# Optimization experiments

Measured on AMD Instinct MI355X. Metric: run time of the kernel, lower is better.

Reference implementation:

```python
import jax, jax.numpy as jnp
import numpy as np

B, L, DIN, H, N, TEMB, NB = 16, 1024, 64, 256, 64, 128, 6


def setup_inputs() -> dict:
    key = jax.random.key(0)
    ks = jax.random.split(key, 16)
    def nrm(k, shape, scale):
        return jax.random.normal(k, shape, dtype=jnp.float32) * scale
    inp = {}
    inp["input"] = nrm(ks[0], (B, L, DIN), 1.0)
    inp["t"] = jax.random.uniform(ks[1], (B,), dtype=jnp.float32) * 1000.0
    inp["W_in"] = nrm(ks[2], (DIN, H), DIN ** -0.5)
    inp["b_in"] = jnp.zeros((H,), jnp.float32)
    inp["Wt1"] = nrm(ks[3], (TEMB, H), TEMB ** -0.5)
    inp["bt1"] = jnp.zeros((H,), jnp.float32)
    inp["Wt2"] = nrm(ks[4], (H, H), H ** -0.5)
    inp["bt2"] = jnp.zeros((H,), jnp.float32)
    inp["ln_g"] = jnp.ones((NB, H), jnp.float32)
    inp["ln_b"] = jnp.zeros((NB, H), jnp.float32)
    lo, hi = float(np.log(0.001)), float(np.log(0.1))
    inp["log_dt"] = jax.random.uniform(ks[5], (NB, H), dtype=jnp.float32) * (hi - lo) + lo
    inp["A_log_re"] = jnp.full((NB, H, N), float(np.log(0.5)), jnp.float32)
    inp["A_im"] = jnp.broadcast_to(np.pi * jnp.arange(N, dtype=jnp.float32), (NB, H, N)) + 0.0
    inp["C_re"] = nrm(ks[6], (NB, 2, H, N), 0.5 ** 0.5)
    inp["C_im"] = nrm(ks[7], (NB, 2, H, N), 0.5 ** 0.5)
    inp["Dp"] = nrm(ks[8], (NB, H), 1.0)
    inp["s4W"] = nrm(ks[9], (NB, H, H), H ** -0.5)
    inp["s4b"] = jnp.zeros((NB, H), jnp.float32)
    inp["tW"] = nrm(ks[10], (NB, H, H), H ** -0.5)
    inp["tb"] = jnp.zeros((NB, H), jnp.float32)
    inp["c1W"] = nrm(ks[11], (NB, H, H), H ** -0.5)
    inp["c1b"] = jnp.zeros((NB, H), jnp.float32)
    inp["c2W"] = nrm(ks[12], (NB, H, H), H ** -0.5)
    inp["c2b"] = jnp.zeros((NB, H), jnp.float32)
    inp["Wo1"] = nrm(ks[13], (H, H), H ** -0.5)
    inp["bo1"] = jnp.zeros((H,), jnp.float32)
    inp["Wo2"] = nrm(ks[14], (H, DIN), H ** -0.5)
    inp["bo2"] = jnp.zeros((DIN,), jnp.float32)
    return inp


def _sin_emb(t, dim):
    half = dim // 2
    freqs = jnp.exp(-np.log(10000.0) / (half - 1) * jnp.arange(half, dtype=jnp.float32))
    a = t[:, None] * freqs[None, :]
    return jnp.concatenate([jnp.sin(a), jnp.cos(a)], axis=-1)


def _forward(input, t, W_in, b_in, Wt1, bt1, Wt2, bt2, ln_g, ln_b, log_dt, A_log_re,
             A_im, C_re, C_im, Dp, s4W, s4b, tW, tb, c1W, c1b, c2W, c2b, Wo1, bo1, Wo2, bo2):
    x = jax.nn.relu(input @ W_in + b_in)                     # [B,L,H]
    tv = jax.nn.silu(_sin_emb(t, TEMB) @ Wt1 + bt1)
    tv = jax.nn.silu(tv @ Wt2 + bt2)                         # [B,H]
    x = jnp.swapaxes(x, -1, -2)                              # [B,H,L]
    length = x.shape[-1]
    nfft = 2 * length
    lgrid = jnp.arange(length)
    skips = jnp.zeros_like(x)
    for i in range(NB):
        # time conditioning (broadcast over L)
        tt = tv @ tW[i] + tb[i]                              # [B,H]
        z = x + tt[:, :, None]
        # LayerNorm over channel dim H
        zt = jnp.swapaxes(z, -1, -2)                         # [B,L,H]
        mu = zt.mean(-1, keepdims=True)
        var = zt.var(-1, keepdims=True)
        zn = (zt - mu) / jnp.sqrt(var + 1e-5) * ln_g[i] + ln_b[i]
        zn = jnp.swapaxes(zn, -1, -2)                        # [B,H,L]
        # S4 (diagonal ZOH) bidirectional convolution kernel
        dt = jnp.exp(log_dt[i])                              # [H]
        A = -jnp.exp(A_log_re[i]) + 1j * A_im[i]             # [H,N]
        dtA = A * dt[:, None]
        C = C_re[i] + 1j * C_im[i]                           # [2,H,N]
        dC = C * (jnp.exp(dtA) - 1.0) / A
        V = jnp.exp(dtA[:, :, None] * lgrid)                 # [H,N,L] Vandermonde
        K = 2.0 * jnp.einsum('shn,hnl->shl', dC, V).real     # [2,H,L]
        k = jnp.pad(K[0], ((0, 0), (0, length))) + jnp.pad(K[1][:, ::-1], ((0, 0), (length, 0)))
        y = jnp.fft.irfft(jnp.fft.rfft(zn, nfft) * jnp.fft.rfft(k, nfft)[None], nfft)[..., :length]
        y = y + zn * Dp[i][None, :, None]
        y = jax.nn.gelu(y, approximate=False)
        y = jnp.einsum('oh,bhl->bol', s4W[i], y) + s4b[i][None, :, None]
        out = y + z                                          # S4Layer residual
        g = jnp.tanh(out) * jax.nn.sigmoid(out)
        x = jnp.einsum('oh,bhl->bol', c1W[i], g) + c1b[i][None, :, None] + x
        skips = skips + jnp.einsum('oh,bhl->bol', c2W[i], g) + c2b[i][None, :, None]
    skip = jnp.swapaxes(skips, -1, -2)                       # [B,L,H]
    h = jax.nn.relu(skip @ Wo1 + bo1)
    out = h @ Wo2 + bo2
    return out + input                                       # init_skip


def reference(input, t, W_in, b_in, Wt1, bt1, Wt2, bt2, ln_g, ln_b, log_dt, A_log_re,
              A_im, C_re, C_im, Dp, s4W, s4b, tW, tb, c1W, c1b, c2W, c2b, Wo1, bo1, Wo2, bo2):
    return _forward(input, t, W_in, b_in, Wt1, bt1, Wt2, bt2, ln_g, ln_b, log_dt, A_log_re,
                    A_im, C_re, C_im, Dp, s4W, s4b, tW, tb, c1W, c1b, c2W, c2b, Wo1, bo1, Wo2, bo2)
```

## Files before the change

### kernel.cpp

```cpp
#include <hip/hip_runtime.h>
#include <math.h>


typedef __attribute__((ext_vector_type(8))) short bf16x8;
typedef __attribute__((ext_vector_type(4))) float f32x4;

__device__ __forceinline__ short f2bf(float f) {
  unsigned u = __builtin_bit_cast(unsigned, f);
  unsigned r = (u + 0x7FFFu + ((u >> 16) & 1u)) >> 16;
  return (short)r;
}
__device__ __forceinline__ float bf2f(unsigned short v) {
  unsigned u = ((unsigned)v) << 16;
  return __builtin_bit_cast(float, u);
}

__global__ __launch_bounds__(256) void k_temb(
    const float* __restrict__ t, const float* __restrict__ Wt1, const float* __restrict__ bt1,
    const float* __restrict__ Wt2, const float* __restrict__ bt2, float* __restrict__ tv) {
  int b = blockIdx.x, tid = threadIdx.x;
  __shared__ float emb[128];
  __shared__ float tv1[256];
  if (tid < 128) {
    int j = tid & 63;
    float f = expf(-logf(10000.f) / 63.f * (float)j);
    float a = t[b] * f;
    emb[tid] = (tid < 64) ? sinf(a) : cosf(a);
  }
  __syncthreads();
  float acc = bt1[tid];
  for (int k = 0; k < 128; k++) acc = fmaf(emb[k], Wt1[k * 256 + tid], acc);
  tv1[tid] = acc / (1.f + expf(-acc));
  __syncthreads();
  float acc2 = bt2[tid];
  for (int k = 0; k < 256; k++) acc2 = fmaf(tv1[k], Wt2[k * 256 + tid], acc2);
  tv[b * 256 + tid] = acc2 / (1.f + expf(-acc2));
}

__global__ __launch_bounds__(256) void k_tt(
    const float* __restrict__ tv, const float* __restrict__ tW, const float* __restrict__ tb,
    float* __restrict__ tt_all) {
  int i = blockIdx.x, b = blockIdx.y, h = threadIdx.x;
  __shared__ float s[256];
  s[h] = tv[b * 256 + h];
  __syncthreads();
  const float* W = tW + i * 256 * 256;
  float acc = tb[i * 256 + h];
  for (int k = 0; k < 256; k++) acc = fmaf(s[k], W[k * 256 + h], acc);
  tt_all[(i * 16 + b) * 256 + h] = acc;
}

__global__ __launch_bounds__(256) void k_in(
    const float* __restrict__ inp, const float* __restrict__ W, const float* __restrict__ bias,
    unsigned short* __restrict__ xbf) {
  int lt = blockIdx.x, b = blockIdx.y, h = threadIdx.x;
  __shared__ float si[64][68];
  int l0 = lt * 64;
  for (int rep = 0; rep < 16; rep++) {
    int idx = rep * 256 + h;
    int l = idx >> 6, d = idx & 63;
    si[l][d] = inp[(size_t)(b * 1024 + l0 + l) * 64 + d];
  }
  float wc[64];
  #pragma unroll
  for (int d = 0; d < 64; d++) wc[d] = W[d * 256 + h];
  float bh = bias[h];
  __syncthreads();
  unsigned short* xp = xbf + (size_t)(b * 256 + h) * 1024 + l0;
  for (int l4 = 0; l4 < 16; l4++) {
    float op[4];
    #pragma unroll
    for (int j = 0; j < 4; j++) {
      int l = l4 * 4 + j;
      float a = bh;
      #pragma unroll
      for (int d4 = 0; d4 < 16; d4++) {
        float4 v = *reinterpret_cast<const float4*>(&si[l][d4 * 4]);
        a = fmaf(v.x, wc[d4 * 4 + 0], a);
        a = fmaf(v.y, wc[d4 * 4 + 1], a);
        a = fmaf(v.z, wc[d4 * 4 + 2], a);
        a = fmaf(v.w, wc[d4 * 4 + 3], a);
      }
      op[j] = fmaxf(a, 0.f);
    }
    ushort4 o = make_ushort4((unsigned short)f2bf(op[0]), (unsigned short)f2bf(op[1]),
                             (unsigned short)f2bf(op[2]), (unsigned short)f2bf(op[3]));
    *reinterpret_cast<ushort4*>(xp + l4 * 4) = o;
  }
}

__global__ __launch_bounds__(256) void k_tab(
    const float* __restrict__ log_dt, const float* __restrict__ A_log_re, const float* __restrict__ A_im,
    const float* __restrict__ C_re, const float* __restrict__ C_im,
    float* __restrict__ wtab, float* __restrict__ wTtab, float* __restrict__ dCtab) {
  int idx = blockIdx.x * 256 + threadIdx.x;
  int i = idx / (256 * 64);
  int rem = idx % (256 * 64);
  int h = rem >> 6, n = rem & 63;
  float dt = expf(log_dt[i * 256 + h]);
  float Ar = -expf(A_log_re[idx]);
  float Ai = A_im[idx];
  float ar = dt * Ar, ai = dt * Ai;
  float ea = expf(ar);
  float wr = ea * cosf(ai), wi = ea * sinf(ai);
  float pr = wr, pi = wi;
  #pragma unroll
  for (int s = 0; s < 6; s++) { float nr = pr * pr - pi * pi; float ni = 2.f * pr * pi; pr = nr; pi = ni; }
  float den = Ar * Ar + Ai * Ai;
  float qr = ((wr - 1.f) * Ar + wi * Ai) / den;
  float qi = (wi * Ar - (wr - 1.f) * Ai) / den;
  wtab[idx * 2] = wr; wtab[idx * 2 + 1] = wi;
  wTtab[idx * 2] = pr; wTtab[idx * 2 + 1] = pi;
  #pragma unroll
  for (int s = 0; s < 2; s++) {
    float cr = C_re[((size_t)(i * 2 + s) * 256 + h) * 64 + n];
    float ci = C_im[((size_t)(i * 2 + s) * 256 + h) * 64 + n];
    dCtab[(((size_t)(i * 2 + s) * 256 + h) * 64 + n) * 2]     = cr * qr - ci * qi;
    dCtab[(((size_t)(i * 2 + s) * 256 + h) * 64 + n) * 2 + 1] = cr * qi + ci * qr;
  }
}

__global__ __launch_bounds__(256) void k_prep(
    const float* __restrict__ s4W, const float* __restrict__ c1W, const float* __restrict__ c2W,
    const float* __restrict__ Wo1,
    unsigned short* __restrict__ s4Wbf, unsigned short* __restrict__ c12Wbf, unsigned short* __restrict__ Wo1T) {
  int idx = blockIdx.x * 256 + threadIdx.x;
  if (idx < 393216) {
    s4Wbf[idx] = (unsigned short)f2bf(s4W[idx]);
  } else if (idx < 393216 + 786432) {
    int j = idx - 393216;
    int i = j / 131072, r = j % 131072;
    int o2 = r >> 8, k = r & 255;
    float v = (o2 < 256) ? c1W[(size_t)i * 65536 + o2 * 256 + k]
                         : c2W[(size_t)i * 65536 + (o2 - 256) * 256 + k];
    c12Wbf[j] = (unsigned short)f2bf(v);
  } else {
    int j = idx - 1179648;
    int o = j >> 8, k = j & 255;
    Wo1T[j] = (unsigned short)f2bf(Wo1[k * 256 + o]);
  }
}

__global__ __launch_bounds__(256) void k_pcar(const float* __restrict__ wtab, unsigned short* __restrict__ Ptb) {
  int idx = blockIdx.x * 256 + threadIdx.x;
  int i = idx >> 14, h = (idx >> 6) & 255, n = idx & 63;
  float wr = wtab[idx * 2], wi = wtab[idx * 2 + 1];
  float pr = 1.f, pi = 0.f;
  unsigned short* base = Ptb + (size_t)i * 2097152 + (size_t)h * 8192 + 2 * n;
  for (int t = 0; t < 64; t++) {
    *reinterpret_cast<ushort2*>(base + t * 128) =
        make_ushort2((unsigned short)f2bf(pr), (unsigned short)f2bf(-pi));
    float nr2 = pr * wr - pi * wi, ni2 = pr * wi + pi * wr;
    pr = nr2; pi = ni2;
  }
}

__global__ __launch_bounds__(256) void k_ktap(
    const float* __restrict__ dCtab, const unsigned short* __restrict__ Ptb, float* __restrict__ Ktap) {
  int idx = blockIdx.x * 256 + threadIdx.x;
  int j = idx & 63;
  int h = (idx >> 6) & 255;
  int i = idx >> 15;
  const float* dc = dCtab + (size_t)(idx >> 6) * 128;
  const unsigned short* P = Ptb + (size_t)i * 2097152 + (size_t)h * 8192 + j * 128;
  float acc = 0.f;
  for (int q = 0; q < 32; q++) {
    float4 d = *reinterpret_cast<const float4*>(dc + q * 4);
    ushort4 p = *reinterpret_cast<const ushort4*>(P + q * 4);
    acc = fmaf(d.x, bf2f(p.x), fmaf(d.y, bf2f(p.y), fmaf(d.z, bf2f(p.z), fmaf(d.w, bf2f(p.w), acc))));
  }
  Ktap[idx] = 2.f * acc;
}

__global__ __launch_bounds__(256) void k_ln(
    const unsigned short* __restrict__ xbf, const float* __restrict__ tt_all,
    const float* __restrict__ g, const float* __restrict__ bta, unsigned short* __restrict__ znbf, int i) {
  int ct = blockIdx.x, b = blockIdx.y, tid = threadIdx.x;
  __shared__ unsigned short tile[64][266];
  __shared__ float stt[256];
  __shared__ float red[8][64];
  __shared__ float mu_s[64], rs_s[64];
  stt[tid] = tt_all[(i * 16 + b) * 256 + tid];
  __syncthreads();
  int l0 = ct * 64;
  const unsigned short* xb = xbf + (size_t)(b * 256) * 1024 + l0;
  for (int rep = 0; rep < 16; rep++) {
    int idx = rep * 256 + tid;
    int h = idx >> 4;
    int l4 = (idx & 15) * 4;
    ushort4 v = *reinterpret_cast<const ushort4*>(xb + (size_t)h * 1024 + l4);
    float a = stt[h];
    tile[l4][h]     = (unsigned short)f2bf(bf2f(v.x) + a);
    tile[l4 + 1][h] = (unsigned short)f2bf(bf2f(v.y) + a);
    tile[l4 + 2][h] = (unsigned short)f2bf(bf2f(v.z) + a);
    tile[l4 + 3][h] = (unsigned short)f2bf(bf2f(v.w) + a);
  }
  __syncthreads();
  int l = tid & 63, part = tid >> 6;
  float s1 = 0.f, s2 = 0.f;
  for (int k = 0; k < 64; k++) {
    float v = bf2f(tile[l][part * 64 + k]);
    s1 += v; s2 = fmaf(v, v, s2);
  }
  red[part][l] = s1; red[4 + part][l] = s2;
  __syncthreads();
  if (tid < 64) {
    float a = red[0][tid] + red[1][tid] + red[2][tid] + red[3][tid];
    float q = red[4][tid] + red[5][tid] + red[6][tid] + red[7][tid];
    float mu = a * (1.f / 256.f);
    float var = q * (1.f / 256.f) - mu * mu;
    mu_s[tid] = mu;
    rs_s[tid] = rsqrtf(var + 1e-5f);
  }
  __syncthreads();
  unsigned short* zb = znbf + (size_t)(b * 256) * 1024 + l0;
  for (int rep = 0; rep < 16; rep++) {
    int idx = rep * 256 + tid;
    int h = idx >> 4;
    int l4 = (idx & 15) * 4;
    float gg = g[i * 256 + h], bb2 = bta[i * 256 + h];
    float o0 = (bf2f(tile[l4][h])     - mu_s[l4])     * rs_s[l4]     * gg + bb2;
    float o1 = (bf2f(tile[l4 + 1][h]) - mu_s[l4 + 1]) * rs_s[l4 + 1] * gg + bb2;
    float o2 = (bf2f(tile[l4 + 2][h]) - mu_s[l4 + 2]) * rs_s[l4 + 2] * gg + bb2;
    float o3 = (bf2f(tile[l4 + 3][h]) - mu_s[l4 + 3]) * rs_s[l4 + 3] * gg + bb2;
    ushort4 o4 = make_ushort4((unsigned short)f2bf(o0), (unsigned short)f2bf(o1),
                              (unsigned short)f2bf(o2), (unsigned short)f2bf(o3));
    *reinterpret_cast<ushort4*>(zb + (size_t)h * 1024 + l4) = o4;
  }
}

__global__ __launch_bounds__(512, 1) void k_s4(
    const unsigned short* __restrict__ znbf, const unsigned short* __restrict__ Ptb,
    const float* __restrict__ wtab, const float* __restrict__ wTtab, const float* __restrict__ dCtab,
    const float* __restrict__ Ktap, const float* __restrict__ Dp,
    unsigned short* __restrict__ ygbf, int i) {
  int h = blockIdx.x;
  int tid = threadIdx.x;
  __shared__ unsigned short Psb[64 * 132];
  __shared__ unsigned short XR[22016];
  __shared__ unsigned short Sw[34816];
  __shared__ float k0s[64], k1s[64];

  if (tid < 64) k0s[tid] = Ktap[h * 64 + tid];
  else if (tid < 128) k1s[tid - 64] = Ktap[16384 + h * 64 + (tid - 64)];

  {
    const unsigned short* src = Ptb + (size_t)h * 8192;
    #pragma unroll
    for (int rep = 0; rep < 4; rep++) {
      int idx4 = (rep * 512 + tid) * 4;
      int t = idx4 >> 7, k = idx4 & 127;
      ushort4 v = *reinterpret_cast<const ushort4*>(src + idx4);
      *reinterpret_cast<ushort4*>(&Psb[t * 132 + k]) = v;
    }
  }
  __syncthreads();
  {
    int t = tid & 63;
    int colblk = tid >> 6;
    #pragma unroll
    for (int cc = 0; cc < 32; cc++) {
      int col = colblk * 32 + cc;
      int n = col & 63, comp = (col >> 6) & 1, dir = col >> 7;
      int k = 2 * n + comp;
      unsigned short v = dir ? Psb[t * 132 + k] : Psb[(63 - t) * 132 + k];
      if (comp) v ^= 0x8000u;
      XR[col * 72 + t] = v;
    }
  }
  __syncthreads();

  int wid = tid >> 6, lane = tid & 63;
  int b = blockIdx.y * 8 + wid;
  int c = lane & 15, kq = lane >> 4;
  const unsigned short* pzn = znbf + ((size_t)(b * 256 + h)) * 1024 + c * 64 + kq * 8;

  bf16x8 af0 = *reinterpret_cast<const bf16x8*>(pzn);
  bf16x8 af1 = *reinterpret_cast<const bf16x8*>(pzn + 32);

  f32x4 acc[16];
  #pragma unroll
  for (int nt = 0; nt < 16; nt++) acc[nt] = (f32x4){0.f, 0.f, 0.f, 0.f};
  #pragma unroll
  for (int nt = 0; nt < 16; nt++) {
    bf16x8 b0 = *reinterpret_cast<const bf16x8*>(&XR[(nt * 16 + c) * 72 + kq * 8]);
    acc[nt] = __builtin_amdgcn_mfma_f32_16x16x32_bf16(af0, b0, acc[nt], 0, 0, 0);
  }
  #pragma unroll
  for (int nt = 0; nt < 16; nt++) {
    bf16x8 b1 = *reinterpret_cast<const bf16x8*>(&XR[(nt * 16 + c) * 72 + 32 + kq * 8]);
    acc[nt] = __builtin_amdgcn_mfma_f32_16x16x32_bf16(af1, b1, acc[nt], 0, 0, 0);
  }
  __syncthreads();

  {
    int trow = tid >> 6, klane = tid & 63;
    #pragma unroll
    for (int ti = 0; ti < 8; ti++) {
      int t2 = ti * 8 + trow;
      #pragma unroll
      for (int kc = 0; kc < 5; kc++) {
        int k = kc * 64 + klane;
        unsigned short v;
        if (kc < 2)      v = Psb[t2 * 132 + k];
        else if (kc < 4) v = Psb[(63 - t2) * 132 + (k - 128)];
        else {
          int tp = klane;
          float f = (t2 >= tp) ? k0s[t2 - tp] : k1s[tp - t2 - 1];
          v = (unsigned short)f2bf(f);
        }
        XR[t2 * 344 + k] = v;
      }
    }
  }

  unsigned short* swf = &Sw[(wid * 2 + 0) * 2176];
  unsigned short* swb = &Sw[(wid * 2 + 1) * 2176];
  const int gib = (i * 256 + h) * 64;
  #pragma unroll
  for (int j = 0; j < 4; j++) {
    int n = j * 16 + c;
    int gi = gib + n;
    float wTr = wTtab[gi * 2], wTi = wTtab[gi * 2 + 1];
    float w2r = wTr * wTr - wTi * wTi, w2i = 2.f * wTr * wTi;
    float w4r = w2r * w2r - w2i * w2i, w4i = 2.f * w2r * w2i;
    float w8r = w4r * w4r - w4i * w4i, w8i = 2.f * w4r * w4i;
    float wr = wtab[gi * 2], wi = wtab[gi * 2 + 1];
    float d0r = dCtab[((size_t)(i * 2 + 0) * 256 + h) * 128 + 2 * n];
    float d0i = dCtab[((size_t)(i * 2 + 0) * 256 + h) * 128 + 2 * n + 1];
    float d1r = dCtab[((size_t)(i * 2 + 1) * 256 + h) * 128 + 2 * n];
    float d1i = dCtab[((size_t)(i * 2 + 1) * 256 + h) * 128 + 2 * n + 1];
    float mfr = 2.f * (d0r * wr - d0i * wi), mfi = 2.f * (d0r * wi + d0i * wr);
    float mbr = 2.f * d1r, mbi = 2.f * d1i;

    {
      float er = 0.f, ei = 0.f, entr[4], enti[4];
      #pragma unroll
      for (int r = 0; r < 4; r++) {
        entr[r] = er; enti[r] = ei;
        float br = acc[j][r], bi = acc[j + 4][r];
        float t0 = er * wTr - ei * wTi + br;
        ei = er * wTi + ei * wTr + bi; er = t0;
      }
      float Gr = er, Gi = ei;
      float sr = __shfl_up(Gr, 16), si = __shfl_up(Gi, 16);
      if (kq >= 1) { Gr += sr * w4r - si * w4i; Gi += sr * w4i + si * w4r; }
      sr = __shfl_up(Gr, 32); si = __shfl_up(Gi, 32);
      if (kq >= 2) { Gr += sr * w8r - si * w8i; Gi += sr * w8i + si * w8r; }
      float Sgr = __shfl_up(Gr, 16), Sgi = __shfl_up(Gi, 16);
      if (kq == 0) { Sgr = 0.f; Sgi = 0.f; }
      float pr = 1.f, pi = 0.f;
      #pragma unroll
      for (int r = 0; r < 4; r++) {
        float scr = pr * Sgr - pi * Sgi + entr[r];
        float sci = pr * Sgi + pi * Sgr + enti[r];
        float opr = mfr * scr - mfi * sci;
        float opi = mfr * sci + mfi * scr;
        *reinterpret_cast<ushort2*>(swf + (kq * 4 + r) * 136 + 2 * n) =
            make_ushort2((unsigned short)f2bf(opr), (unsigned short)f2bf(opi));
        float t0 = pr * wTr - pi * wTi; pi = pr * wTi + pi * wTr; pr = t0;
      }
    }
    {
      float er = 0.f, ei = 0.f, entr[4], enti[4];
      #pragma unroll
      for (int rr = 0; rr < 4; rr++) {
        int r = 3 - rr;
        entr[r] = er; enti[r] = ei;
        float br = acc[8 + j][r], bi = acc[12 + j][r];
        float t0 = er * wTr - ei * wTi + br;
        ei = er * wTi + ei * wTr + bi; er = t0;
      }
      float Gr = er, Gi = ei;
      float sr = __shfl_down(Gr, 16), si = __shfl_down(Gi, 16);
      if (kq <= 2) { Gr += sr * w4r - si * w4i; Gi += sr * w4i + si * w4r; }
      sr = __shfl_down(Gr, 32); si = __shfl_down(Gi, 32);
      if (kq <= 1) { Gr += sr * w8r - si * w8i; Gi += sr * w8i + si * w8r; }
      float Sgr = __shfl_down(Gr, 16), Sgi = __shfl_down(Gi, 16);
      if (kq == 3) { Sgr = 0.f; Sgi = 0.f; }
      float pr = 1.f, pi = 0.f;
      #pragma unroll
      for (int rr = 0; rr < 4; rr++) {
        int r = 3 - rr;
        float scr = pr * Sgr - pi * Sgi + entr[r];
        float sci = pr * Sgi + pi * Sgr + enti[r];
        float opr = mbr * scr - mbi * sci;
        float opi = mbr * sci + mbi * scr;
        *reinterpret_cast<ushort2*>(swb + (kq * 4 + r) * 136 + 2 * n) =
            make_ushort2((unsigned short)f2bf(opr), (unsigned short)f2bf(opi));
        float t0 = pr * wTr - pi * wTi; pi = pr * wTi + pi * wTr; pr = t0;
      }
    }
  }
  __syncthreads();

  f32x4 acc2[4];
  #pragma unroll
  for (int nt = 0; nt < 4; nt++) acc2[nt] = (f32x4){0.f, 0.f, 0.f, 0.f};
  #pragma unroll
  for (int ks = 0; ks < 10; ks++) {
    bf16x8 af;
    if (ks < 4)       af = *reinterpret_cast<const bf16x8*>(swf + c * 136 + ks * 32 + kq * 8);
    else if (ks < 8)  af = *reinterpret_cast<const bf16x8*>(swb + c * 136 + (ks - 4) * 32 + kq * 8);
    else              af = *reinterpret_cast<const bf16x8*>(pzn + (ks - 8) * 32);
    #pragma unroll
    for (int nt = 0; nt < 4; nt++) {
      bf16x8 bfv = *reinterpret_cast<const bf16x8*>(&XR[(nt * 16 + c) * 344 + ks * 32 + kq * 8]);
      acc2[nt] = __builtin_amdgcn_mfma_f32_16x16x32_bf16(af, bfv, acc2[nt], 0, 0, 0);
    }
  }

  float dp = Dp[i * 256 + h];
  size_t obase = (size_t)(b * 256 + h) * 1024;
  #pragma unroll
  for (int nt = 0; nt < 4; nt++) {
    #pragma unroll
    for (int r = 0; r < 4; r++) {
      int m = kq * 4 + r;
      int t = nt * 16 + c;
      size_t idx = obase + (size_t)m * 64 + t;
      float z = bf2f(znbf[idx]);
      float v = fmaf(z, dp, acc2[nt][r]);
      float gel = 0.5f * v * (1.f + erff(v * 0.70710678118f));
      ygbf[idx] = (unsigned short)f2bf(gel);
    }
  }
}

template <int EPI>
__global__ __launch_bounds__(256) void k_gemm(
    const unsigned short* __restrict__ Wbf, const float* __restrict__ bias1, const float* __restrict__ bias2,
    const unsigned short* __restrict__ act, unsigned short* __restrict__ uio1, unsigned short* __restrict__ uio2,
    unsigned short* __restrict__ outb, const unsigned short* __restrict__ aux1, const float* __restrict__ aux2) {
  int lt = blockIdx.x, ot = blockIdx.y, b = blockIdx.z;
  int tid = threadIdx.x;
  int l0 = lt * 128, o0 = ot * 64;
  __shared__ unsigned short Alds[128 * 40];

  int wid = tid >> 6, lane = tid & 63;
  int wo = wid >> 1, wl = wid & 1;
  int c = lane & 15, kq = lane >> 4;

  int kq4 = tid >> 5;
  int lq = tid & 31;
  const unsigned short* actb = act + (size_t)(b * 256) * 1024 + l0 + lq * 4;

  f32x4 acc[2][4];
  #pragma unroll
  for (int mo = 0; mo < 2; mo++)
    #pragma unroll
    for (int nl = 0; nl < 4; nl++) acc[mo][nl] = (f32x4){0.f, 0.f, 0.f, 0.f};

  ushort4 m0, m1, m2, m3;
  {
    const unsigned short* p = actb + (size_t)(kq4 * 4) * 1024;
    m0 = *reinterpret_cast<const ushort4*>(p);
    m1 = *reinterpret_cast<const ushort4*>(p + 1024);
    m2 = *reinterpret_cast<const ushort4*>(p + 2048);
    m3 = *reinterpret_cast<const ushort4*>(p + 3072);
  }

  for (int kc = 0; kc < 256; kc += 32) {
    {
      int g0 = kq4 >> 1, hh = (kq4 & 1) * 4;
      int rot = (g0 + lq) & 3;
      unsigned short* wp = &Alds[(lq * 4) * 40 + rot * 8 + hh];
      ushort4 w;
      w = make_ushort4(m0.x, m1.x, m2.x, m3.x); *reinterpret_cast<ushort4*>(wp) = w;
      w = make_ushort4(m0.y, m1.y, m2.y, m3.y); *reinterpret_cast<ushort4*>(wp + 40) = w;
      w = make_ushort4(m0.z, m1.z, m2.z, m3.z); *reinterpret_cast<ushort4*>(wp + 80) = w;
      w = make_ushort4(m0.w, m1.w, m2.w, m3.w); *reinterpret_cast<ushort4*>(wp + 120) = w;
    }
    __syncthreads();
    {
      int kcn = (kc + 32) & 255;
      const unsigned short* p = actb + (size_t)(kcn + kq4 * 4) * 1024;
      m0 = *reinterpret_cast<const ushort4*>(p);
      m1 = *reinterpret_cast<const ushort4*>(p + 1024);
      m2 = *reinterpret_cast<const ushort4*>(p + 2048);
      m3 = *reinterpret_cast<const ushort4*>(p + 3072);
    }
    bf16x8 af[2];
    #pragma unroll
    for (int mo = 0; mo < 2; mo++) {
      const unsigned short* wp = Wbf + (size_t)(o0 + wo * 32 + mo * 16 + c) * 256 + kc + kq * 8;
      af[mo] = *reinterpret_cast<const bf16x8*>(wp);
    }
    bf16x8 bfr[4];
    #pragma unroll
    for (int nl = 0; nl < 4; nl++) {
      int l = wl * 64 + nl * 16 + c;
      int rot = (kq + (l >> 2)) & 3;
      bfr[nl] = *reinterpret_cast<const bf16x8*>(&Alds[l * 40 + rot * 8]);
    }
    #pragma unroll
    for (int mo = 0; mo < 2; mo++)
      #pragma unroll
      for (int nl = 0; nl < 4; nl++)
        acc[mo][nl] = __builtin_amdgcn_mfma_f32_16x16x32_bf16(af[mo], bfr[nl], acc[mo][nl], 0, 0, 0);
    __syncthreads();
  }

  #pragma unroll
  for (int mo = 0; mo < 2; mo++) {
    #pragma unroll
    for (int nl = 0; nl < 4; nl++) {
      #pragma unroll
      for (int r = 0; r < 4; r++) {
        float a = acc[mo][nl][r];
        int o = o0 + wo * 32 + mo * 16 + kq * 4 + r;
        int l = l0 + wl * 64 + nl * 16 + c;
        if constexpr (EPI == 0) {
          size_t id = ((size_t)(b * 256 + o)) * 1024 + l;
          float u = a + bias1[o] + bf2f(aux1[id]) + aux2[b * 256 + o];
          float t = __expf(fminf(-u, 80.f));
          float gg = (1.f - t) / (1.f + t * t);
          outb[id] = (unsigned short)f2bf(gg);
        } else if constexpr (EPI == 1 || EPI == 4) {
          if (o < 256) {
            size_t id = ((size_t)(b * 256 + o)) * 1024 + l;
            uio1[id] = (unsigned short)f2bf(bf2f(uio1[id]) + a + bias1[o]);
          } else {
            int o2 = o - 256;
            size_t id = ((size_t)(b * 256 + o2)) * 1024 + l;
            if constexpr (EPI == 4) uio2[id] = (unsigned short)f2bf(a + bias2[o2]);
            else                    uio2[id] = (unsigned short)f2bf(bf2f(uio2[id]) + a + bias2[o2]);
          }
        } else {
          size_t id = ((size_t)(b * 256 + o)) * 1024 + l;
          outb[id] = (unsigned short)f2bf(fmaxf(a + bias1[o], 0.f));
        }
      }
    }
  }
}

__global__ __launch_bounds__(256) void k_out(
    const unsigned short* __restrict__ h1, const float* __restrict__ Wo2, const float* __restrict__ bo2,
    const float* __restrict__ inp, float* __restrict__ outp) {
  int lt = blockIdx.x, b = blockIdx.y, tid = threadIdx.x;
  __shared__ float sa[32][132];
  __shared__ float sw2[32][68];
  int l0 = lt * 128;
  float acc[4][8];
  #pragma unroll
  for (int r = 0; r < 4; r++)
    #pragma unroll
    for (int c2 = 0; c2 < 8; c2++) acc[r][c2] = 0.f;
  int df = (tid & 7) * 8;
  int lf = (tid >> 3) * 4;
  for (int kc = 0; kc < 256; kc += 32) {
    for (int rep = 0; rep < 4; rep++) {
      int idx = rep * 256 + tid;
      int kk = idx >> 5;
      int l4 = (idx & 31) * 4;
      ushort4 v = *reinterpret_cast<const ushort4*>(h1 + (size_t)(b * 256 + kc + kk) * 1024 + l0 + l4);
      sa[kk][l4] = bf2f(v.x); sa[kk][l4 + 1] = bf2f(v.y);
      sa[kk][l4 + 2] = bf2f(v.z); sa[kk][l4 + 3] = bf2f(v.w);
    }
    for (int rep = 0; rep < 8; rep++) {
      int idx = rep * 256 + tid;
      int kk = idx >> 6, d = idx & 63;
      sw2[kk][d] = Wo2[(size_t)(kc + kk) * 64 + d];
    }
    __syncthreads();
    for (int kk = 0; kk < 32; kk++) {
      float4 av = *reinterpret_cast<const float4*>(&sa[kk][lf]);
      float4 w1 = *reinterpret_cast<const float4*>(&sw2[kk][df]);
      float4 w2 = *reinterpret_cast<const float4*>(&sw2[kk][df + 4]);
      float avv[4] = {av.x, av.y, av.z, av.w};
      float wv[8] = {w1.x, w1.y, w1.z, w1.w, w2.x, w2.y, w2.z, w2.w};
      #pragma unroll
      for (int r = 0; r < 4; r++)
        #pragma unroll
        for (int c2 = 0; c2 < 8; c2++) acc[r][c2] = fmaf(avv[r], wv[c2], acc[r][c2]);
    }
    __syncthreads();
  }
  float bv[8];
  #pragma unroll
  for (int c2 = 0; c2 < 8; c2++) bv[c2] = bo2[df + c2];
  #pragma unroll
  for (int r = 0; r < 4; r++) {
    size_t base = (size_t)(b * 1024 + l0 + lf + r) * 64 + df;
    float4 i1 = *reinterpret_cast<const float4*>(inp + base);
    float4 i2 = *reinterpret_cast<const float4*>(inp + base + 4);
    float4 o1 = make_float4(acc[r][0] + bv[0] + i1.x, acc[r][1] + bv[1] + i1.y,
                            acc[r][2] + bv[2] + i1.z, acc[r][3] + bv[3] + i1.w);
    float4 o2 = make_float4(acc[r][4] + bv[4] + i2.x, acc[r][5] + bv[5] + i2.y,
                            acc[r][6] + bv[6] + i2.z, acc[r][7] + bv[7] + i2.w);
    *reinterpret_cast<float4*>(outp + base) = o1;
    *reinterpret_cast<float4*>(outp + base + 4) = o2;
  }
}

extern "C" void kernel_launch(void* const* d_in, const int* in_sizes, int n_in,
                              void* d_out, int out_size, void* d_ws, size_t ws_size,
                              hipStream_t stream) {
  const float* input   = (const float*)d_in[0];
  const float* t       = (const float*)d_in[1];
  const float* W_in    = (const float*)d_in[2];
  const float* b_in    = (const float*)d_in[3];
  const float* Wt1     = (const float*)d_in[4];
  const float* bt1     = (const float*)d_in[5];
  const float* Wt2     = (const float*)d_in[6];
  const float* bt2     = (const float*)d_in[7];
  const float* ln_g    = (const float*)d_in[8];
  const float* ln_b    = (const float*)d_in[9];
  const float* log_dt  = (const float*)d_in[10];
  const float* A_log_re= (const float*)d_in[11];
  const float* A_im    = (const float*)d_in[12];
  const float* C_re    = (const float*)d_in[13];
  const float* C_im    = (const float*)d_in[14];
  const float* Dp      = (const float*)d_in[15];
  const float* s4W     = (const float*)d_in[16];
  const float* s4b     = (const float*)d_in[17];
  const float* tW      = (const float*)d_in[18];
  const float* tb      = (const float*)d_in[19];
  const float* c1W     = (const float*)d_in[20];
  const float* c1b     = (const float*)d_in[21];
  const float* c2W     = (const float*)d_in[22];
  const float* c2b     = (const float*)d_in[23];
  const float* Wo1     = (const float*)d_in[24];
  const float* bo1     = (const float*)d_in[25];
  const float* Wo2     = (const float*)d_in[26];
  const float* bo2     = (const float*)d_in[27];

  float* ws = (float*)d_ws;
  size_t off = 0;
  float* xbuf   = ws + off; off += 4194304;
  float* znbuf  = ws + off; off += 4194304;
  float* ygbuf  = ws + off; off += 4194304;
  float* skbuf  = ws + off; off += 4194304;
  float* tv     = ws + off; off += 4096;
  float* tt_all = ws + off; off += 24576;
  float* wtab   = ws + off; off += 196608;
  float* wTtab  = ws + off; off += 196608;
  float* dCtab  = ws + off; off += 393216;
  float* Ptbuf  = ws + off; off += 6291456;
  float* Ktap   = ws + off; off += 196608;
  unsigned short* s4Wbf  = (unsigned short*)(ws + off); off += 196608;
  unsigned short* c12Wbf = (unsigned short*)(ws + off); off += 393216;
  unsigned short* Wo1T   = (unsigned short*)(ws + off); off += 32768;

  unsigned short* xbf     = (unsigned short*)xbuf;
  unsigned short* znbf    = (unsigned short*)znbuf;
  unsigned short* ygbf    = (unsigned short*)ygbuf;
  unsigned short* gbf     = (unsigned short*)(ygbuf + 2097152);
  unsigned short* skipsbf = (unsigned short*)skbuf;
  unsigned short* Ptb     = (unsigned short*)Ptbuf;
  unsigned short* h1bf    = (unsigned short*)znbuf;

  k_temb<<<16, 256, 0, stream>>>(t, Wt1, bt1, Wt2, bt2, tv);
  k_tt<<<dim3(6, 16), 256, 0, stream>>>(tv, tW, tb, tt_all);
  k_in<<<dim3(16, 16), 256, 0, stream>>>(input, W_in, b_in, xbf);
  k_tab<<<384, 256, 0, stream>>>(log_dt, A_log_re, A_im, C_re, C_im, wtab, wTtab, dCtab);
  k_prep<<<4864, 256, 0, stream>>>(s4W, c1W, c2W, Wo1, s4Wbf, c12Wbf, Wo1T);
  k_pcar<<<384, 256, 0, stream>>>(wtab, Ptb);
  k_ktap<<<768, 256, 0, stream>>>(dCtab, Ptb, Ktap);

  for (int i = 0; i < 6; i++) {
    k_ln<<<dim3(16, 16), 256, 0, stream>>>(xbf, tt_all, ln_g, ln_b, znbf, i);
    k_s4<<<dim3(256, 2), 512, 0, stream>>>(znbf, Ptb + (size_t)i * 2097152, wtab, wTtab, dCtab,
                                           Ktap + (size_t)i * 32768, Dp, ygbf, i);
    k_gemm<0><<<dim3(8, 4, 16), 256, 0, stream>>>(s4Wbf + (size_t)i * 65536, s4b + i * 256, nullptr,
                                                  ygbf, nullptr, nullptr, gbf, xbf, tt_all + i * 4096);
    if (i == 0)
      k_gemm<4><<<dim3(8, 8, 16), 256, 0, stream>>>(c12Wbf, c1b, c2b, gbf, xbf, skipsbf,
                                                    nullptr, nullptr, nullptr);
    else
      k_gemm<1><<<dim3(8, 8, 16), 256, 0, stream>>>(c12Wbf + (size_t)i * 131072, c1b + i * 256,
                                                    c2b + i * 256, gbf, xbf, skipsbf,
                                                    nullptr, nullptr, nullptr);
  }
  k_gemm<2><<<dim3(8, 4, 16), 256, 0, stream>>>(Wo1T, bo1, nullptr,
                                                skipsbf, nullptr, nullptr, h1bf, nullptr, nullptr);
  k_out<<<dim3(8, 16), 256, 0, stream>>>(h1bf, Wo2, bo2, input, (float*)d_out);
}
```

Baseline: 514.4 us.

## Double output tile per GEMM block, use tanh-form GELU, vectorize LN reads

Each GEMM block now computes two 64-row output tiles from the same staged activation tile, which halves the grid and the repeated global reads and LDS transposes of activations. For the c1/c2 GEMM the two tiles are the matching c1 and c2 rows, so both paths share one pass over the gated input. The exact erf GELU in the S4 kernel is replaced by the tanh approximation written as a sigmoid with fast exp, changing numerics slightly. LayerNorm statistics read bf16 pairs instead of single values. The larger tile doubles accumulator registers and halves the block count, which may reduce occupancy.

```diff
diff --git a/kernel.cpp b/kernel.cpp
--- a/kernel.cpp
+++ b/kernel.cpp
@@ -13,6 +13,10 @@
 __device__ __forceinline__ float bf2f(unsigned short v) {
   unsigned u = ((unsigned)v) << 16;
   return __builtin_bit_cast(float, u);
+}
+__device__ __forceinline__ float gelu_f(float v) {
+  float q = 1.5957691216f * v * fmaf(0.044715f, v * v, 1.f);
+  return v / (1.f + __expf(-q));
 }
 
 __global__ __launch_bounds__(256) void k_temb(
@@ -198,9 +202,11 @@
   __syncthreads();
   int l = tid & 63, part = tid >> 6;
   float s1 = 0.f, s2 = 0.f;
-  for (int k = 0; k < 64; k++) {
-    float v = bf2f(tile[l][part * 64 + k]);
-    s1 += v; s2 = fmaf(v, v, s2);
+  for (int k2 = 0; k2 < 32; k2++) {
+    ushort2 v2 = *reinterpret_cast<const ushort2*>(&tile[l][part * 64 + k2 * 2]);
+    float a = bf2f(v2.x), bq = bf2f(v2.y);
+    s1 += a + bq;
+    s2 = fmaf(a, a, fmaf(bq, bq, s2));
   }
   red[part][l] = s1; red[4 + part][l] = s2;
   __syncthreads();
@@ -421,8 +427,7 @@
       size_t idx = obase + (size_t)m * 64 + t;
       float z = bf2f(znbf[idx]);
       float v = fmaf(z, dp, acc2[nt][r]);
-      float gel = 0.5f * v * (1.f + erff(v * 0.70710678118f));
-      ygbf[idx] = (unsigned short)f2bf(gel);
+      ygbf[idx] = (unsigned short)f2bf(gelu_f(v));
     }
   }
 }
@@ -431,10 +436,11 @@
 __global__ __launch_bounds__(256) void k_gemm(
     const unsigned short* __restrict__ Wbf, const float* __restrict__ bias1, const float* __restrict__ bias2,
     const unsigned short* __restrict__ act, unsigned short* __restrict__ uio1, unsigned short* __restrict__ uio2,
-    unsigned short* __restrict__ outb, const unsigned short* __restrict__ aux1, const float* __restrict__ aux2) {
+    unsigned short* __restrict__ outb, const unsigned short* __restrict__ aux1, const float* __restrict__ aux2,
+    int obm, int ot2s) {
   int lt = blockIdx.x, ot = blockIdx.y, b = blockIdx.z;
   int tid = threadIdx.x;
-  int l0 = lt * 128, o0 = ot * 64;
+  int l0 = lt * 128;
   __shared__ unsigned short Alds[128 * 40];
 
   int wid = tid >> 6, lane = tid & 63;
@@ -445,11 +451,13 @@
   int lq = tid & 31;
   const unsigned short* actb = act + (size_t)(b * 256) * 1024 + l0 + lq * 4;
 
-  f32x4 acc[2][4];
-  #pragma unroll
-  for (int mo = 0; mo < 2; mo++)
-    #pragma unroll
-    for (int nl = 0; nl < 4; nl++) acc[mo][nl] = (f32x4){0.f, 0.f, 0.f, 0.f};
+  f32x4 acc[2][2][4];
+  #pragma unroll
+  for (int ot2 = 0; ot2 < 2; ot2++)
+    #pragma unroll
+    for (int mo = 0; mo < 2; mo++)
+      #pragma unroll
+      for (int nl = 0; nl < 4; nl++) acc[ot2][mo][nl] = (f32x4){0.f, 0.f, 0.f, 0.f};
 
   ushort4 m0, m1, m2, m3;
   {
@@ -480,12 +488,6 @@
       m2 = *reinterpret_cast<const ushort4*>(p + 2048);
       m3 = *reinterpret_cast<const ushort4*>(p + 3072);
     }
-    bf16x8 af[2];
-    #pragma unroll
-    for (int mo = 0; mo < 2; mo++) {
-      const unsigned short* wp = Wbf + (size_t)(o0 + wo * 32 + mo * 16 + c) * 256 + kc + kq * 8;
-      af[mo] = *reinterpret_cast<const bf16x8*>(wp);
-    }
     bf16x8 bfr[4];
     #pragma unroll
     for (int nl = 0; nl < 4; nl++) {
@@ -494,41 +496,55 @@
       bfr[nl] = *reinterpret_cast<const bf16x8*>(&Alds[l * 40 + rot * 8]);
     }
     #pragma unroll
-    for (int mo = 0; mo < 2; mo++)
-      #pragma unroll
-      for (int nl = 0; nl < 4; nl++)
-        acc[mo][nl] = __builtin_amdgcn_mfma_f32_16x16x32_bf16(af[mo], bfr[nl], acc[mo][nl], 0, 0, 0);
+    for (int ot2 = 0; ot2 < 2; ot2++) {
+      int o0 = ot * obm + ot2 * ot2s;
+      bf16x8 af[2];
+      #pragma unroll
+      for (int mo = 0; mo < 2; mo++) {
+        const unsigned short* wp = Wbf + (size_t)(o0 + wo * 32 + mo * 16 + c) * 256 + kc + kq * 8;
+        af[mo] = *reinterpret_cast<const bf16x8*>(wp);
+      }
+      #pragma unroll
+      for (int mo = 0; mo < 2; mo++)
+        #pragma unroll
+        for (int nl = 0; nl < 4; nl++)
+          acc[ot2][mo][nl] = __builtin_amdgcn_mfma_f32_16x16x32_bf16(af[mo], bfr[nl], acc[ot2][mo][nl], 0, 0, 0);
+    }
     __syncthreads();
   }
 
   #pragma unroll
-  for (int mo = 0; mo < 2; mo++) {
-    #pragma unroll
-    for (int nl = 0; nl < 4; nl++) {
-      #pragma unroll
-      for (int r = 0; r < 4; r++) {
-        float a = acc[mo][nl][r];
-        int o = o0 + wo * 32 + mo * 16 + kq * 4 + r;
-        int l = l0 + wl * 64 + nl * 16 + c;
-        if constexpr (EPI == 0) {
-          size_t id = ((size_t)(b * 256 + o)) * 1024 + l;
-          float u = a + bias1[o] + bf2f(aux1[id]) + aux2[b * 256 + o];
-          float t = __expf(fminf(-u, 80.f));
-          float gg = (1.f - t) / (1.f + t * t);
-          outb[id] = (unsigned short)f2bf(gg);
-        } else if constexpr (EPI == 1 || EPI == 4) {
-          if (o < 256) {
+  for (int ot2 = 0; ot2 < 2; ot2++) {
+    int o0 = ot * obm + ot2 * ot2s;
+    #pragma unroll
+    for (int mo = 0; mo < 2; mo++) {
+      #pragma unroll
+      for (int nl = 0; nl < 4; nl++) {
+        #pragma unroll
+        for (int r = 0; r < 4; r++) {
+          float a = acc[ot2][mo][nl][r];
+          int o = o0 + wo * 32 + mo * 16 + kq * 4 + r;
+          int l = l0 + wl * 64 + nl * 16 + c;
+          if constexpr (EPI == 0) {
             size_t id = ((size_t)(b * 256 + o)) * 1024 + l;
-            uio1[id] = (unsigned short)f2bf(bf2f(uio1[id]) + a + bias1[o]);
+            float u = a + bias1[o] + bf2f(aux1[id]) + aux2[b * 256 + o];
+            float t = __expf(fminf(-u, 80.f));
+            float gg = (1.f - t) / (1.f + t * t);
+            outb[id] = (unsigned short)f2bf(gg);
+          } else if constexpr (EPI == 1 || EPI == 4) {
+            if (o < 256) {
+              size_t id = ((size_t)(b * 256 + o)) * 1024 + l;
+              uio1[id] = (unsigned short)f2bf(bf2f(uio1[id]) + a + bias1[o]);
+            } else {
+              int o2 = o - 256;
+              size_t id = ((size_t)(b * 256 + o2)) * 1024 + l;
+              if constexpr (EPI == 4) uio2[id] = (unsigned short)f2bf(a + bias2[o2]);
+              else                    uio2[id] = (unsigned short)f2bf(bf2f(uio2[id]) + a + bias2[o2]);
+            }
           } else {
-            int o2 = o - 256;
-            size_t id = ((size_t)(b * 256 + o2)) * 1024 + l;
-            if constexpr (EPI == 4) uio2[id] = (unsigned short)f2bf(a + bias2[o2]);
-            else                    uio2[id] = (unsigned short)f2bf(bf2f(uio2[id]) + a + bias2[o2]);
+            size_t id = ((size_t)(b * 256 + o)) * 1024 + l;
+            outb[id] = (unsigned short)f2bf(fmaxf(a + bias1[o], 0.f));
           }
-        } else {
-          size_t id = ((size_t)(b * 256 + o)) * 1024 + l;
-          outb[id] = (unsigned short)f2bf(fmaxf(a + bias1[o], 0.f));
         }
       }
     }
@@ -663,17 +679,19 @@
     k_ln<<<dim3(16, 16), 256, 0, stream>>>(xbf, tt_all, ln_g, ln_b, znbf, i);
     k_s4<<<dim3(256, 2), 512, 0, stream>>>(znbf, Ptb + (size_t)i * 2097152, wtab, wTtab, dCtab,
                                            Ktap + (size_t)i * 32768, Dp, ygbf, i);
-    k_gemm<0><<<dim3(8, 4, 16), 256, 0, stream>>>(s4Wbf + (size_t)i * 65536, s4b + i * 256, nullptr,
-                                                  ygbf, nullptr, nullptr, gbf, xbf, tt_all + i * 4096);
+    k_gemm<0><<<dim3(8, 2, 16), 256, 0, stream>>>(s4Wbf + (size_t)i * 65536, s4b + i * 256, nullptr,
+                                                  ygbf, nullptr, nullptr, gbf, xbf, tt_all + i * 4096,
+                                                  128, 64);
     if (i == 0)
-      k_gemm<4><<<dim3(8, 8, 16), 256, 0, stream>>>(c12Wbf, c1b, c2b, gbf, xbf, skipsbf,
-                                                    nullptr, nullptr, nullptr);
+      k_gemm<4><<<dim3(8, 4, 16), 256, 0, stream>>>(c12Wbf, c1b, c2b, gbf, xbf, skipsbf,
+                                                    nullptr, nullptr, nullptr, 64, 256);
     else
-      k_gemm<1><<<dim3(8, 8, 16), 256, 0, stream>>>(c12Wbf + (size_t)i * 131072, c1b + i * 256,
+      k_gemm<1><<<dim3(8, 4, 16), 256, 0, stream>>>(c12Wbf + (size_t)i * 131072, c1b + i * 256,
                                                     c2b + i * 256, gbf, xbf, skipsbf,
-                                                    nullptr, nullptr, nullptr);
-  }
-  k_gemm<2><<<dim3(8, 4, 16), 256, 0, stream>>>(Wo1T, bo1, nullptr,
-                                                skipsbf, nullptr, nullptr, h1bf, nullptr, nullptr);
+                                                    nullptr, nullptr, nullptr, 64, 256);
+  }
+  k_gemm<2><<<dim3(8, 2, 16), 256, 0, stream>>>(Wo1T, bo1, nullptr,
+                                                skipsbf, nullptr, nullptr, h1bf, nullptr, nullptr,
+                                                128, 64);
   k_out<<<dim3(8, 16), 256, 0, stream>>>(h1bf, Wo2, bo2, input, (float*)d_out);
 }
```

Measured after the change: 629.6 us. 22.4% more time.
